# Kernel optimization log

Measured on AMD Instinct MI355X. Metric: run time of the kernel, lower is better.

Reference implementation:

```python
import jax, jax.numpy as jnp
import numpy as np

B, T, D, H = 4, 2048, 1024, 16
HD = D // H  # head_dim = 64

def setup_inputs() -> dict:
    key = jax.random.key(0)
    k1, k2, k3 = jax.random.split(key, 3)
    x = jax.random.normal(k1, (B, T, D), dtype=jnp.float32)
    w_qkv = jax.random.normal(k2, (D, 3 * D), dtype=jnp.float32) * (D ** -0.5)
    b_qkv = jnp.zeros((3 * D,), dtype=jnp.float32)
    w_proj = jax.random.normal(k3, (D, D), dtype=jnp.float32) * (D ** -0.5)
    b_proj = jnp.zeros((D,), dtype=jnp.float32)
    return {"x": x, "w_qkv": w_qkv, "b_qkv": b_qkv, "w_proj": w_proj, "b_proj": b_proj}

def reference(x, w_qkv, b_qkv, w_proj, b_proj):
    b, t, d = x.shape
    scale = HD ** -0.5
    qkv = x @ w_qkv + b_qkv                          # [B,T,3D]
    qkv = qkv.reshape(b, t, 3, H, HD)
    qkv = jnp.transpose(qkv, (2, 0, 3, 1, 4))        # [3,B,H,T,HD]
    q, k, v = qkv[0], qkv[1], qkv[2]
    att = jnp.einsum("bhqd,bhkd->bhqk", q, k) * scale  # [B,H,T,T]
    mask = jnp.tril(jnp.ones((t, t), dtype=att.dtype))[None, None]
    att = att * mask + (1.0 - mask) * (-1e9)
    att = jax.nn.softmax(att, axis=-1)
    # dropout inactive (training=False)
    y = jnp.einsum("bhqk,bhkd->bhqd", att, v)        # [B,H,T,HD]
    y = jnp.transpose(y, (0, 2, 1, 3)).reshape(b, t, d)
    return y @ w_proj + b_proj
```

## Files before the change

### kernel.cpp

```cpp
#include <hip/hip_runtime.h>
#include <hip/hip_bf16.h>

typedef unsigned short u16;
typedef short short8 __attribute__((ext_vector_type(8)));
typedef short bf16x4 __attribute__((ext_vector_type(4)));
typedef float f32x4 __attribute__((ext_vector_type(4)));
typedef float f32x16 __attribute__((ext_vector_type(16)));

#define B_SZ 4
#define T_SEQ 2048
#define DMODEL 1024
#define NH 16
#define HD 64
#define QKV_ELEMS 8388608ull
#define QSCALE (0.125f * 1.44269504f)

__device__ __forceinline__ u16 f2bf(float f) {
    __hip_bfloat16 h = __float2bfloat16(f);
    return __builtin_bit_cast(u16, h);
}

__device__ __forceinline__ void gload16(const void* g, void* l) {
    __builtin_amdgcn_global_load_lds(
        (const __attribute__((address_space(1))) unsigned int*)g,
        (__attribute__((address_space(3))) unsigned int*)l, 16, 0, 0);
}

__global__ __launch_bounds__(256) void cast_x_kernel(
    const float4* __restrict__ x, u16* __restrict__ xb)
{
    const int i = blockIdx.x * 256 + threadIdx.x;
    const float4 v = x[i];
    union { u16 u[4]; uint2 d; } p;
    p.u[0] = f2bf(v.x); p.u[1] = f2bf(v.y); p.u[2] = f2bf(v.z); p.u[3] = f2bf(v.w);
    *(uint2*)(xb + (size_t)i * 4) = p.d;
}

__global__ __launch_bounds__(256) void tcast_kernel(
    const float* __restrict__ w, u16* __restrict__ wt, int K, int N)
{
    const int n = blockIdx.x * 256 + threadIdx.x;
    const int k0 = blockIdx.y * 256;
    for (int kk = 0; kk < 256; kk += 8) {
        short8 o;
#pragma unroll
        for (int e = 0; e < 8; ++e)
            o[e] = (short)f2bf(w[(size_t)(k0 + kk + e) * N + n]);
        *(short8*)&wt[(size_t)n * K + k0 + kk] = o;
    }
}

template <int EPI>
__global__ __launch_bounds__(256) void gemm_kernel(
    const u16* __restrict__ A, const u16* __restrict__ Bt,
    const float* __restrict__ bias, void* __restrict__ outp)
{
    __shared__ u16 As[128 * 64];
    __shared__ u16 Bs[128 * 64];
    const int tid = threadIdx.x;
    const int l = tid & 63;
    const int w = tid >> 6;
    const int wm = w >> 1, wn = w & 1;
    const int m0 = blockIdx.y * 128, n0 = blockIdx.x * 128;
    const int srow = l >> 3;
    const int sch  = (l & 7) ^ srow;
    const int fr = l & 15, fq = l >> 4;

    f32x4 acc[4][4] = {};

    for (int k0 = 0; k0 < 1024; k0 += 64) {
        __syncthreads();
#pragma unroll
        for (int ii = 0; ii < 4; ++ii) {
            const int row = w * 32 + ii * 8;
            gload16(&A[(size_t)(m0 + row + srow) * 1024 + k0 + sch * 8], &As[row * 64]);
            gload16(&Bt[(size_t)(n0 + row + srow) * 1024 + k0 + sch * 8], &Bs[row * 64]);
        }
        __syncthreads();
#pragma unroll
        for (int ks = 0; ks < 2; ++ks) {
            short8 af[4], bf[4];
#pragma unroll
            for (int t = 0; t < 4; ++t) {
                const int ar = wm * 64 + t * 16 + fr;
                af[t] = *(const short8*)&As[ar * 64 + (((ks * 4 + fq) ^ (l & 7)) << 3)];
                const int br = wn * 64 + t * 16 + fr;
                bf[t] = *(const short8*)&Bs[br * 64 + (((ks * 4 + fq) ^ (l & 7)) << 3)];
            }
#pragma unroll
            for (int mt = 0; mt < 4; ++mt)
#pragma unroll
                for (int nt = 0; nt < 4; ++nt)
                    acc[mt][nt] = __builtin_amdgcn_mfma_f32_16x16x32_bf16(
                        af[mt], bf[nt], acc[mt][nt], 0, 0, 0);
        }
    }

    if (EPI == 0) {
        u16* qkv = (u16*)outp;
#pragma unroll
        for (int nt = 0; nt < 4; ++nt) {
            const int n = n0 + wn * 64 + nt * 16 + fr;
            const float bs = bias[n];
            const int which = n >> 10, hh = (n >> 6) & 15, d = n & 63;
            if (which == 2) {
                u16* dst = qkv + 2 * QKV_ELEMS;
#pragma unroll
                for (int mt = 0; mt < 4; ++mt) {
                    const int m = m0 + wm * 64 + mt * 16 + fq * 4;
                    const int bb = m >> 11, t = m & 2047;
                    bf16x4 ov;
#pragma unroll
                    for (int r = 0; r < 4; ++r) ov[r] = (short)f2bf(acc[mt][nt][r] + bs);
                    *(bf16x4*)&dst[(((size_t)(bb * NH + hh)) * HD + d) * T_SEQ + t] = ov;
                }
            } else {
                const float scl = (which == 0) ? QSCALE : 1.0f;
                u16* dst = qkv + (size_t)which * QKV_ELEMS + (size_t)hh * T_SEQ * HD + d;
#pragma unroll
                for (int mt = 0; mt < 4; ++mt)
#pragma unroll
                    for (int r = 0; r < 4; ++r) {
                        const int m = m0 + wm * 64 + mt * 16 + fq * 4 + r;
                        const int bb = m >> 11, t = m & 2047;
                        dst[(size_t)bb * (NH * T_SEQ * HD) + (size_t)t * HD] =
                            f2bf((acc[mt][nt][r] + bs) * scl);
                    }
            }
        }
    } else {
        float* C = (float*)outp;
#pragma unroll
        for (int nt = 0; nt < 4; ++nt) {
            const int n = n0 + wn * 64 + nt * 16 + fr;
            const float bs = bias[n];
#pragma unroll
            for (int mt = 0; mt < 4; ++mt)
#pragma unroll
                for (int r = 0; r < 4; ++r) {
                    const int m = m0 + wm * 64 + mt * 16 + fq * 4 + r;
                    C[(size_t)m * DMODEL + n] = acc[mt][nt][r] + bs;
                }
        }
    }
}

__global__ __launch_bounds__(256) void attn_kernel(
    const u16* __restrict__ q, const u16* __restrict__ k,
    const u16* __restrict__ vT, u16* __restrict__ y)
{
    __shared__ u16 Ks[2][64 * 64];
    __shared__ u16 Vs[2][64 * 64];

    int flat = blockIdx.x;
    flat = (flat & 7) * 64 + (flat >> 3);
    const int qip = flat & 7;
    const int hh = (flat >> 3) & 15;
    const int bb = flat >> 7;

    const size_t hbase = ((size_t)(bb * NH + hh)) * T_SEQ * HD;
    const u16* qb = q + hbase;
    const u16* kb = k + hbase;
    const u16* vTb = vT + hbase;

    const int tid = threadIdx.x;
    const int l = tid & 63;
    const int w = tid >> 6;
    const int qn = l & 31;
    const int h = l >> 5;
    const int srow = l >> 3;
    const int sch = (l & 7) ^ srow;

    u16* Qstage = &Ks[0][0];

    for (int pp = 0; pp < 2; ++pp) {
        const int qi = pp ? (15 - qip) : qip;
        const int q0 = qi * 128;

        __syncthreads();

#pragma unroll
        for (int ii = 0; ii < 4; ++ii) {
            const int row = w * 32 + ii * 8;
            gload16(&qb[(size_t)(q0 + row + srow) * HD + sch * 8], &Qstage[row * 64]);
        }
        {
            const int row = w * 16, row2 = w * 16 + 8;
            gload16(&vTb[(size_t)(row + srow) * T_SEQ + sch * 8], &Vs[0][row * 64]);
            gload16(&vTb[(size_t)(row2 + srow) * T_SEQ + sch * 8], &Vs[0][row2 * 64]);
        }
        __syncthreads();

        short8 qf[4];
        {
            const int qrow = w * 32 + qn;
#pragma unroll
            for (int k16 = 0; k16 < 4; ++k16)
                qf[k16] = *(const short8*)
                    &Qstage[qrow * 64 + (((k16 * 2 + h) ^ (qrow & 7)) << 3)];
        }
        __syncthreads();

        {
            const int row = w * 16, row2 = w * 16 + 8;
            gload16(&kb[(size_t)(row + srow) * HD + sch * 8], &Ks[0][row * 64]);
            gload16(&kb[(size_t)(row2 + srow) * HD + sch * 8], &Ks[0][row2 * 64]);
        }

        const int q0w = q0 + w * 32;
        float l_run = 0.f;
        f32x16 o_acc[2] = {};

        const int nkt = 2 * (qi + 1);
        for (int kt = 0; kt < nkt; ++kt) {
            __syncthreads();
            if (kt + 1 < nkt) {
                const int nb = (kt + 1) & 1;
                const int jj = (kt + 1) * 64;
                const int row = w * 16, row2 = w * 16 + 8;
                gload16(&kb[(size_t)(jj + row + srow) * HD + sch * 8],
                        &Ks[nb][row * 64]);
                gload16(&kb[(size_t)(jj + row2 + srow) * HD + sch * 8],
                        &Ks[nb][row2 * 64]);
                gload16(&vTb[(size_t)(row + srow) * T_SEQ + jj + sch * 8],
                        &Vs[nb][row * 64]);
                gload16(&vTb[(size_t)(row2 + srow) * T_SEQ + jj + sch * 8],
                        &Vs[nb][row2 * 64]);
            }
            const int buf = kt & 1;
            const int j0 = kt * 64;

            if (j0 > q0w + 31) continue;
            const int njt = (j0 + 32 <= q0w + 31) ? 2 : 1;

            f32x16 st[2];
#pragma unroll
            for (int jt = 0; jt < 2; ++jt) {
                if (jt >= njt) continue;
                f32x16 s;
#pragma unroll
                for (int r = 0; r < 16; ++r) s[r] = -16.f;
#pragma unroll
                for (int k16 = 0; k16 < 4; ++k16) {
                    const int jrow = jt * 32 + qn;
                    const short8 kf = *(const short8*)
                        &Ks[buf][jrow * 64 + (((k16 * 2 + h) ^ (jrow & 7)) << 3)];
                    s = __builtin_amdgcn_mfma_f32_32x32x16_bf16(kf, qf[k16], s, 0, 0, 0);
                }
                st[jt] = s;
            }

            const int qg = q0w + qn;
#pragma unroll
            for (int jt = 0; jt < 2; ++jt) {
                if (jt >= njt) continue;
                const bool needMask = (j0 + jt * 32 + 31) > q0w;
                if (needMask) {
#pragma unroll
                    for (int r = 0; r < 16; ++r) {
                        const int jg = j0 + jt * 32 + (r & 3) + 8 * (r >> 2) + 4 * h;
                        if (jg > qg) st[jt][r] = -1e30f;
                    }
                }
            }

            float ls = 0.f;
#pragma unroll
            for (int jt = 0; jt < 2; ++jt) {
                if (jt >= njt) continue;
                float s0 = 0.f, s1 = 0.f, s2 = 0.f, s3 = 0.f;
#pragma unroll
                for (int r = 0; r < 16; r += 4) {
                    float p0 = exp2f(st[jt][r]);
                    float p1 = exp2f(st[jt][r + 1]);
                    float p2 = exp2f(st[jt][r + 2]);
                    float p3 = exp2f(st[jt][r + 3]);
                    st[jt][r] = p0; st[jt][r + 1] = p1;
                    st[jt][r + 2] = p2; st[jt][r + 3] = p3;
                    s0 += p0; s1 += p1; s2 += p2; s3 += p3;
                }
                ls += (s0 + s1) + (s2 + s3);
            }
            ls += __shfl_xor(ls, 32);
            l_run += ls;

#pragma unroll
            for (int jt = 0; jt < 2; ++jt) {
                if (jt >= njt) continue;
#pragma unroll
                for (int g = 0; g < 4; ++g) {
                    bf16x4 pk;
#pragma unroll
                    for (int e = 0; e < 4; ++e) pk[e] = (short)f2bf(st[jt][g * 4 + e]);
#pragma unroll
                    for (int dt = 0; dt < 2; ++dt) {
                        const int drow = dt * 32 + qn;
                        const bf16x4 vf = *(const bf16x4*)
                            &Vs[buf][drow * 64 +
                                     (((jt * 4 + g) ^ (drow & 7)) << 3) + h * 4];
                        o_acc[dt] = __builtin_amdgcn_mfma_f32_32x32x8bf16_1k(
                            vf, pk, o_acc[dt], 0, 0, 0);
                    }
                }
            }
        }

        const float inv = 1.f / l_run;
        const int t = q0w + qn;
        u16* yrow = y + ((size_t)(bb * T_SEQ + t)) * DMODEL + hh * HD;
#pragma unroll
        for (int dt = 0; dt < 2; ++dt)
#pragma unroll
            for (int g = 0; g < 4; ++g) {
                bf16x4 ov;
#pragma unroll
                for (int e = 0; e < 4; ++e)
                    ov[e] = (short)f2bf(o_acc[dt][g * 4 + e] * inv);
                *(bf16x4*)&yrow[dt * 32 + g * 8 + h * 4] = ov;
            }
    }
}

extern "C" void kernel_launch(void* const* d_in, const int* in_sizes, int n_in,
                              void* d_out, int out_size, void* d_ws, size_t ws_size,
                              hipStream_t stream) {
    const float* x      = (const float*)d_in[0];
    const float* w_qkv  = (const float*)d_in[1];
    const float* b_qkv  = (const float*)d_in[2];
    const float* w_proj = (const float*)d_in[3];
    const float* b_proj = (const float*)d_in[4];
    float* out = (float*)d_out;

    u16* xb  = (u16*)d_ws;
    u16* wqT = xb + 8388608;
    u16* wpT = wqT + 3145728;
    u16* qkv = wpT + 1048576;
    u16* yb  = qkv + 3 * QKV_ELEMS;

    cast_x_kernel<<<8192, 256, 0, stream>>>((const float4*)x, xb);
    tcast_kernel<<<dim3(12, 4), 256, 0, stream>>>(w_qkv, wqT, 1024, 3072);
    tcast_kernel<<<dim3(4, 4), 256, 0, stream>>>(w_proj, wpT, 1024, 1024);
    gemm_kernel<0><<<dim3(24, 64), 256, 0, stream>>>(xb, wqT, b_qkv, (void*)qkv);
    attn_kernel<<<dim3(512), 256, 0, stream>>>(
        qkv, qkv + QKV_ELEMS, qkv + 2 * QKV_ELEMS, yb);
    gemm_kernel<1><<<dim3(8, 64), 256, 0, stream>>>(yb, wpT, b_proj, (void*)out);
}
```

Measured before the change: 315.1 us.

## Merge cast/transpose prep kernels into one launch and add MFMA priority hints

The three preprocessing kernels (x cast, w_qkv transpose-cast, w_proj transpose-cast) become one prep kernel whose block ranges pick the task. The weight transposes now run on more, smaller blocks (64-row K chunks), which gives more parallelism. This removes two launches and the tail idle time between them. The attention kernel also wraps its QK and PV MFMA loops with s_setprio to favour matrix issue across waves, and computes the output row index from q0 and the wave id instead of q0w.

New measurement: 285.1 us. 9.5% less time.

```diff
diff --git a/kernel.cpp b/kernel.cpp
--- a/kernel.cpp
+++ b/kernel.cpp
@@ -26,27 +26,45 @@
         (__attribute__((address_space(3))) unsigned int*)l, 16, 0, 0);
 }
 
-__global__ __launch_bounds__(256) void cast_x_kernel(
-    const float4* __restrict__ x, u16* __restrict__ xb)
+#define NCX 2048
+__global__ __launch_bounds__(256) void prep_kernel(
+    const float4* __restrict__ x, u16* __restrict__ xb,
+    const float* __restrict__ w_qkv, u16* __restrict__ wqT,
+    const float* __restrict__ w_proj, u16* __restrict__ wpT)
 {
-    const int i = blockIdx.x * 256 + threadIdx.x;
-    const float4 v = x[i];
-    union { u16 u[4]; uint2 d; } p;
-    p.u[0] = f2bf(v.x); p.u[1] = f2bf(v.y); p.u[2] = f2bf(v.z); p.u[3] = f2bf(v.w);
-    *(uint2*)(xb + (size_t)i * 4) = p.d;
-}
-
-__global__ __launch_bounds__(256) void tcast_kernel(
-    const float* __restrict__ w, u16* __restrict__ wt, int K, int N)
-{
-    const int n = blockIdx.x * 256 + threadIdx.x;
-    const int k0 = blockIdx.y * 256;
-    for (int kk = 0; kk < 256; kk += 8) {
-        short8 o;
-#pragma unroll
-        for (int e = 0; e < 8; ++e)
-            o[e] = (short)f2bf(w[(size_t)(k0 + kk + e) * N + n]);
-        *(short8*)&wt[(size_t)n * K + k0 + kk] = o;
+    const int b = blockIdx.x;
+    if (b < NCX) {
+        int i = b * 256 + threadIdx.x;
+#pragma unroll
+        for (int rep = 0; rep < 4; ++rep, i += NCX * 256) {
+            const float4 v = x[i];
+            union { u16 u[4]; uint2 d; } p;
+            p.u[0] = f2bf(v.x); p.u[1] = f2bf(v.y);
+            p.u[2] = f2bf(v.z); p.u[3] = f2bf(v.w);
+            *(uint2*)(xb + (size_t)i * 4) = p.d;
+        }
+    } else if (b < NCX + 192) {
+        const int bb2 = b - NCX;
+        const int n = (bb2 % 12) * 256 + threadIdx.x;
+        const int k0 = (bb2 / 12) * 64;
+        for (int kk = 0; kk < 64; kk += 8) {
+            short8 o;
+#pragma unroll
+            for (int e = 0; e < 8; ++e)
+                o[e] = (short)f2bf(w_qkv[(size_t)(k0 + kk + e) * 3072 + n]);
+            *(short8*)&wqT[(size_t)n * 1024 + k0 + kk] = o;
+        }
+    } else {
+        const int bb2 = b - NCX - 192;
+        const int n = (bb2 % 4) * 256 + threadIdx.x;
+        const int k0 = (bb2 / 4) * 64;
+        for (int kk = 0; kk < 64; kk += 8) {
+            short8 o;
+#pragma unroll
+            for (int e = 0; e < 8; ++e)
+                o[e] = (short)f2bf(w_proj[(size_t)(k0 + kk + e) * 1024 + n]);
+            *(short8*)&wpT[(size_t)n * 1024 + k0 + kk] = o;
+        }
     }
 }
 
@@ -234,6 +252,7 @@
             const int njt = (j0 + 32 <= q0w + 31) ? 2 : 1;
 
             f32x16 st[2];
+            __builtin_amdgcn_s_setprio(1);
 #pragma unroll
             for (int jt = 0; jt < 2; ++jt) {
                 if (jt >= njt) continue;
@@ -249,6 +268,7 @@
                 }
                 st[jt] = s;
             }
+            __builtin_amdgcn_s_setprio(0);
 
             const int qg = q0w + qn;
 #pragma unroll
@@ -284,6 +304,7 @@
             ls += __shfl_xor(ls, 32);
             l_run += ls;
 
+            __builtin_amdgcn_s_setprio(1);
 #pragma unroll
             for (int jt = 0; jt < 2; ++jt) {
                 if (jt >= njt) continue;
@@ -303,10 +324,11 @@
                     }
                 }
             }
+            __builtin_amdgcn_s_setprio(0);
         }
 
         const float inv = 1.f / l_run;
-        const int t = q0w + qn;
+        const int t = q0 + w * 32 + qn;
         u16* yrow = y + ((size_t)(bb * T_SEQ + t)) * DMODEL + hh * HD;
 #pragma unroll
         for (int dt = 0; dt < 2; ++dt)
@@ -337,9 +359,8 @@
     u16* qkv = wpT + 1048576;
     u16* yb  = qkv + 3 * QKV_ELEMS;
 
-    cast_x_kernel<<<8192, 256, 0, stream>>>((const float4*)x, xb);
-    tcast_kernel<<<dim3(12, 4), 256, 0, stream>>>(w_qkv, wqT, 1024, 3072);
-    tcast_kernel<<<dim3(4, 4), 256, 0, stream>>>(w_proj, wpT, 1024, 1024);
+    prep_kernel<<<2304, 256, 0, stream>>>((const float4*)x, xb,
+                                          w_qkv, wqT, w_proj, wpT);
     gemm_kernel<0><<<dim3(24, 64), 256, 0, stream>>>(xb, wqT, b_qkv, (void*)qkv);
     attn_kernel<<<dim3(512), 256, 0, stream>>>(
         qkv, qkv + QKV_ELEMS, qkv + 2 * QKV_ELEMS, yb);
```
